# Kernel optimization log

Hardware: AMD Instinct MI355X
Metric: run time of the kernel (lower is better)

## Reference

```python
import jax, jax.numpy as jnp
import numpy as np


def setup_inputs() -> dict:
    key = jax.random.key(0)
    k1, k2, k3, k4 = jax.random.split(key, 4)
    B, T, N, C_IN, C_OUT, K = 32, 24, 1024, 64, 64, 3
    x = jax.random.normal(k1, (B, T, N, C_IN), dtype=jnp.float32)
    Tks = jax.random.normal(k2, (K, N, N), dtype=jnp.float32)
    # kaiming-uniform-ish init scale for Theta, small uniform bias
    bound_t = float(np.sqrt(6.0 / C_IN))
    Theta = jax.random.uniform(k3, (K, C_IN, C_OUT), dtype=jnp.float32,
                               minval=-bound_t, maxval=bound_t)
    bound_b = 1.0 / float(np.sqrt(C_IN))
    bias = jax.random.uniform(k4, (K, C_OUT), dtype=jnp.float32,
                              minval=-bound_b, maxval=bound_b)
    return {"x": x, "Tks": Tks, "Theta": Theta, "bias": bias}


def reference(x, Tks, Theta, bias):
    # torch.einsum('nn,btnc->btnc', T_k, x) extracts diag(T_k) and scales x per node.
    d = jnp.diagonal(Tks, axis1=1, axis2=2)  # [K, N]
    # sum_k diag(T_k) * x @ Theta_k  -> [B, T, N, C_OUT]
    out = jnp.einsum('kn,btnc,kco->btno', d, x, Theta)
    # each bias[k] is added once -> total additive term is sum over k
    out = out + jnp.sum(bias, axis=0)
    return out
```

## Files before the change

kernel.cpp:

```cpp
#include <hip/hip_runtime.h>


#define NNODES 1024
#define TILE_ROWS 64
#define NT 8
#define ROWS_PER_BLOCK (TILE_ROWS * NT)
#define NBLOCKS (786432 / ROWS_PER_BLOCK)

#define WS_W  0
#define WS_BS (24 * 1024)
#define WS_DV (24 * 1024 + 256)

typedef __attribute__((ext_vector_type(8))) short short8;
typedef __attribute__((ext_vector_type(4))) float f32x4;
typedef __attribute__((ext_vector_type(4))) int   i32x4;

__device__ __forceinline__ unsigned short f2bf(float f) {
    union { float f; unsigned u; } v; v.f = f;
    unsigned r = v.u + 0x7FFFu + ((v.u >> 16) & 1u);
    return (unsigned short)(r >> 16);
}

__device__ __forceinline__ int cvt_pk_bf16(float lo, float hi) {
    int r;
    asm("v_cvt_pk_bf16_f32 %0, %1, %2" : "=v"(r) : "v"(lo), "v"(hi));
    return r;
}

__device__ __forceinline__ void gload_lds16(const void* g, void* l) {
    __builtin_amdgcn_global_load_lds(
        (const __attribute__((address_space(1))) void*)g,
        (__attribute__((address_space(3))) void*)l,
        16, 0, 0);
}

__global__ void cheb_prep(const float* __restrict__ Tks,
                          const float* __restrict__ Theta,
                          const float* __restrict__ bias,
                          unsigned char* __restrict__ ws) {
    const int b = blockIdx.x;
    const int l = threadIdx.x;
    if (b < 24) {
        const int kc = b >> 3, h = (b >> 2) & 1, nb = b & 3;
        const int o  = nb * 16 + (l & 15);
        const int cb = h * 32 + (l >> 4) * 8;
        unsigned short* dst = (unsigned short*)(ws + WS_W) + ((size_t)b * 64 + l) * 8;
        #pragma unroll
        for (int j = 0; j < 8; ++j)
            dst[j] = f2bf(Theta[kc * 4096 + (cb + j) * 64 + o]);
    } else if (b < 40) {
        const int n = (b - 24) * 64 + l;
        const size_t dg = (size_t)n * (NNODES + 1);
        f32x4 v;
        v[0] = Tks[dg];
        v[1] = Tks[(size_t)NNODES * NNODES + dg];
        v[2] = Tks[(size_t)2 * NNODES * NNODES + dg];
        v[3] = 0.0f;
        *((f32x4*)(ws + WS_DV) + n) = v;
    } else {
        float* bs = (float*)(ws + WS_BS);
        bs[l] = bias[l] + bias[64 + l] + bias[128 + l];
    }
}

__global__ __launch_bounds__(256) void cheb_main(
    const float* __restrict__ x,
    const unsigned char* __restrict__ ws,
    float* __restrict__ out)
{
    __shared__ float xs[4][TILE_ROWS * 64];

    const int tid  = threadIdx.x;
    const int wave = tid >> 6;
    const int lane = tid & 63;
    const int lrow = lane & 15;
    const int lgrp = lane >> 4;
    const size_t rowbase = (size_t)blockIdx.x * ROWS_PER_BLOCK;

    const unsigned short* wimg = (const unsigned short*)(ws + WS_W);
    const float*          bsum = (const float*)(ws + WS_BS);
    const f32x4*          dvec = (const f32x4*)(ws + WS_DV);

    short8 wf[3][2][4];
    #pragma unroll
    for (int kc = 0; kc < 3; ++kc)
        #pragma unroll
        for (int h = 0; h < 2; ++h)
            #pragma unroll
            for (int nb = 0; nb < 4; ++nb)
                wf[kc][h][nb] = *(const short8*)(
                    wimg + ((size_t)(((kc * 2 + h) * 4 + nb) * 64 + lane)) * 8);

    f32x4 bs4[4];
    #pragma unroll
    for (int nb = 0; nb < 4; ++nb)
        bs4[nb] = *(const f32x4*)(bsum + nb * 16 + lgrp * 4);

    f32x4 dvr[NT];
    #pragma unroll
    for (int t = 0; t < NT; ++t)
        dvr[t] = dvec[(rowbase + t * TILE_ROWS + wave * 16 + lrow) & (NNODES - 1)];

#define STAGE(T) do { if ((T) < NT) {                                         \
        _Pragma("unroll")                                                     \
        for (int s = 0; s < 4; ++s) {                                         \
            const int u_ = wave * 4 + s;                                      \
            const int R_ = u_ * 4 + lgrp;                                     \
            const int c_ = (lrow * 16) ^ ((R_ & 7) << 4);                     \
            const char* g_ = (const char*)x +                                 \
                (((rowbase + (size_t)(T) * TILE_ROWS + R_) << 8) + c_);       \
            gload_lds16(g_, &xs[(T) & 3][u_ * 256]);                          \
        } } } while (0)

#define WAITV(N) do {                                                         \
        asm volatile("s_waitcnt vmcnt(" #N ")" ::: "memory");                 \
        __builtin_amdgcn_sched_barrier(0);                                    \
    } while (0)

#define BODY(T) do {                                                          \
        const int R = wave * 16 + lrow;                                       \
        const int m_ = (lrow & 7) << 4;                                       \
        const char* rowp = (const char*)&xs[(T) & 3][R * 64];                 \
        const int c00 = (lgrp * 32) ^ m_;                                     \
        const int c01 = (lgrp * 32 + 16) ^ m_;                                \
        const f32x4 x0 = *(const f32x4*)(rowp + c00);                         \
        const f32x4 x1 = *(const f32x4*)(rowp + c01);                         \
        const f32x4 x2 = *(const f32x4*)(rowp + 128 + c00);                   \
        const f32x4 x3 = *(const f32x4*)(rowp + 128 + c01);                   \
        const f32x4 dv = dvr[T];                                              \
        short8 xf[3][2];                                                      \
        _Pragma("unroll")                                                     \
        for (int kc = 0; kc < 3; ++kc) {                                      \
            const float dk = dv[kc];                                          \
            i32x4 r0, r1;                                                     \
            r0[0] = cvt_pk_bf16(dk * x0[0], dk * x0[1]);                      \
            r0[1] = cvt_pk_bf16(dk * x0[2], dk * x0[3]);                      \
            r0[2] = cvt_pk_bf16(dk * x1[0], dk * x1[1]);                      \
            r0[3] = cvt_pk_bf16(dk * x1[2], dk * x1[3]);                      \
            r1[0] = cvt_pk_bf16(dk * x2[0], dk * x2[1]);                      \
            r1[1] = cvt_pk_bf16(dk * x2[2], dk * x2[3]);                      \
            r1[2] = cvt_pk_bf16(dk * x3[0], dk * x3[1]);                      \
            r1[3] = cvt_pk_bf16(dk * x3[2], dk * x3[3]);                      \
            xf[kc][0] = __builtin_bit_cast(short8, r0);                       \
            xf[kc][1] = __builtin_bit_cast(short8, r1);                       \
        }                                                                     \
        f32x4 acc[4] = {f32x4{0,0,0,0}, f32x4{0,0,0,0},                       \
                        f32x4{0,0,0,0}, f32x4{0,0,0,0}};                      \
        _Pragma("unroll")                                                     \
        for (int kc = 0; kc < 3; ++kc)                                        \
            _Pragma("unroll")                                                 \
            for (int h = 0; h < 2; ++h)                                       \
                _Pragma("unroll")                                             \
                for (int nb = 0; nb < 4; ++nb)                                \
                    acc[nb] = __builtin_amdgcn_mfma_f32_16x16x32_bf16(        \
                        wf[kc][h][nb], xf[kc][h], acc[nb], 0, 0, 0);          \
        float* orow = out + (rowbase + (size_t)(T) * TILE_ROWS + R) * 64;     \
        _Pragma("unroll")                                                     \
        for (int nb = 0; nb < 4; ++nb) {                                      \
            f32x4 o4;                                                         \
            _Pragma("unroll")                                                 \
            for (int j = 0; j < 4; ++j) o4[j] = acc[nb][j] + bs4[nb][j];      \
            *(f32x4*)(orow + nb * 16 + lgrp * 4) = o4;                        \
        }                                                                     \
    } while (0)

    STAGE(0); STAGE(1); STAGE(2);
    STAGE(3);  WAITV(12); BODY(0);
    STAGE(4);  WAITV(16); BODY(1);
    STAGE(5);  WAITV(20); BODY(2);
    STAGE(6);  WAITV(24); BODY(3);
    STAGE(7);  WAITV(24); BODY(4);
    STAGE(8);  WAITV(20); BODY(5);
    STAGE(9);  WAITV(16); BODY(6);
    STAGE(10); WAITV(12); BODY(7);

#undef STAGE
#undef WAITV
#undef BODY
}

extern "C" void kernel_launch(void* const* d_in, const int* in_sizes, int n_in,
                              void* d_out, int out_size, void* d_ws, size_t ws_size,
                              hipStream_t stream) {
    const float* x     = (const float*)d_in[0];
    const float* Tks   = (const float*)d_in[1];
    const float* Theta = (const float*)d_in[2];
    const float* bias  = (const float*)d_in[3];
    float* out = (float*)d_out;
    unsigned char* ws = (unsigned char*)d_ws;

    hipLaunchKernelGGL(cheb_prep, dim3(41), dim3(64), 0, stream,
                       Tks, Theta, bias, ws);
    hipLaunchKernelGGL(cheb_main, dim3(NBLOCKS), dim3(256), 0, stream,
                       x, ws, out);
}
```

Baseline: 95.81 us.

## Split output columns across wave pairs with shared LDS tiles and barriers

The block grows from 256 to 512 threads. Each pair of waves now shares one 16-row x tile in LDS and splits the 64 output columns, so each wave holds half the Theta fragments and issues half the MFMAs. The LDS ring drops from four to three buffers, and the per-row diagonal scales are loaded asynchronously into LDS instead of per-thread registers. This lowers register pressure and raises occupancy for a bandwidth-bound kernel. In exchange it adds a workgroup barrier per tile, and both waves of a pair redo the same bf16 conversion.

```diff
diff --git a/kernel.cpp b/kernel.cpp
--- a/kernel.cpp
+++ b/kernel.cpp
@@ -63,71 +63,74 @@
     }
 }
 
-__global__ __launch_bounds__(256) void cheb_main(
+__global__ __launch_bounds__(512, 4) void cheb_main(
     const float* __restrict__ x,
     const unsigned char* __restrict__ ws,
     float* __restrict__ out)
 {
-    __shared__ float xs[4][TILE_ROWS * 64];
+    __shared__ float xs[3][TILE_ROWS * 64];
+    __shared__ __align__(16) float dvs[ROWS_PER_BLOCK][4];
 
     const int tid  = threadIdx.x;
     const int wave = tid >> 6;
     const int lane = tid & 63;
     const int lrow = lane & 15;
     const int lgrp = lane >> 4;
+    const int wr   = wave >> 1;
+    const int q    = wave & 1;
     const size_t rowbase = (size_t)blockIdx.x * ROWS_PER_BLOCK;
 
     const unsigned short* wimg = (const unsigned short*)(ws + WS_W);
     const float*          bsum = (const float*)(ws + WS_BS);
     const f32x4*          dvec = (const f32x4*)(ws + WS_DV);
 
-    short8 wf[3][2][4];
+    short8 wf[3][2][2];
     #pragma unroll
     for (int kc = 0; kc < 3; ++kc)
         #pragma unroll
         for (int h = 0; h < 2; ++h)
             #pragma unroll
-            for (int nb = 0; nb < 4; ++nb)
+            for (int nb = 0; nb < 2; ++nb)
                 wf[kc][h][nb] = *(const short8*)(
-                    wimg + ((size_t)(((kc * 2 + h) * 4 + nb) * 64 + lane)) * 8);
+                    wimg + ((size_t)(((kc * 2 + h) * 4 + q * 2 + nb) * 64 + lane)) * 8);
 
-    f32x4 bs4[4];
+    f32x4 bs4[2];
     #pragma unroll
-    for (int nb = 0; nb < 4; ++nb)
-        bs4[nb] = *(const f32x4*)(bsum + nb * 16 + lgrp * 4);
+    for (int nb = 0; nb < 2; ++nb)
+        bs4[nb] = *(const f32x4*)(bsum + q * 32 + nb * 16 + lgrp * 4);
 
-    f32x4 dvr[NT];
-    #pragma unroll
-    for (int t = 0; t < NT; ++t)
-        dvr[t] = dvec[(rowbase + t * TILE_ROWS + wave * 16 + lrow) & (NNODES - 1)];
+    gload_lds16((const char*)dvec + (((rowbase + wave * 64) & (NNODES - 1)) * 16 + lane * 16),
+                &dvs[wave * 64][0]);
 
 #define STAGE(T) do { if ((T) < NT) {                                         \
         _Pragma("unroll")                                                     \
-        for (int s = 0; s < 4; ++s) {                                         \
-            const int u_ = wave * 4 + s;                                      \
+        for (int s = 0; s < 2; ++s) {                                         \
+            const int u_ = wave * 2 + s;                                      \
             const int R_ = u_ * 4 + lgrp;                                     \
             const int c_ = (lrow * 16) ^ ((R_ & 7) << 4);                     \
             const char* g_ = (const char*)x +                                 \
                 (((rowbase + (size_t)(T) * TILE_ROWS + R_) << 8) + c_);       \
-            gload_lds16(g_, &xs[(T) & 3][u_ * 256]);                          \
+            gload_lds16(g_, (char*)&xs[(T) % 3][0] + u_ * 1024);              \
         } } } while (0)
 
 #define WAITV(N) do {                                                         \
         asm volatile("s_waitcnt vmcnt(" #N ")" ::: "memory");                 \
         __builtin_amdgcn_sched_barrier(0);                                    \
+        __builtin_amdgcn_s_barrier();                                         \
+        __builtin_amdgcn_sched_barrier(0);                                    \
     } while (0)
 
 #define BODY(T) do {                                                          \
-        const int R = wave * 16 + lrow;                                       \
+        const int R = wr * 16 + lrow;                                         \
         const int m_ = (lrow & 7) << 4;                                       \
-        const char* rowp = (const char*)&xs[(T) & 3][R * 64];                 \
+        const char* rowp = (const char*)&xs[(T) % 3][0] + R * 256;            \
         const int c00 = (lgrp * 32) ^ m_;                                     \
         const int c01 = (lgrp * 32 + 16) ^ m_;                                \
         const f32x4 x0 = *(const f32x4*)(rowp + c00);                         \
         const f32x4 x1 = *(const f32x4*)(rowp + c01);                         \
         const f32x4 x2 = *(const f32x4*)(rowp + 128 + c00);                   \
         const f32x4 x3 = *(const f32x4*)(rowp + 128 + c01);                   \
-        const f32x4 dv = dvr[T];                                              \
+        const f32x4 dv = *(const f32x4*)(&dvs[(T) * TILE_ROWS + R][0]);       \
         short8 xf[3][2];                                                      \
         _Pragma("unroll")                                                     \
         for (int kc = 0; kc < 3; ++kc) {                                      \
@@ -144,19 +147,19 @@
             xf[kc][0] = __builtin_bit_cast(short8, r0);                       \
             xf[kc][1] = __builtin_bit_cast(short8, r1);                       \
         }                                                                     \
-        f32x4 acc[4] = {f32x4{0,0,0,0}, f32x4{0,0,0,0},                       \
-                        f32x4{0,0,0,0}, f32x4{0,0,0,0}};                      \
+        f32x4 acc[2] = {f32x4{0,0,0,0}, f32x4{0,0,0,0}};                      \
         _Pragma("unroll")                                                     \
         for (int kc = 0; kc < 3; ++kc)                                        \
             _Pragma("unroll")                                                 \
             for (int h = 0; h < 2; ++h)                                       \
                 _Pragma("unroll")                                             \
-                for (int nb = 0; nb < 4; ++nb)                                \
+                for (int nb = 0; nb < 2; ++nb)                                \
                     acc[nb] = __builtin_amdgcn_mfma_f32_16x16x32_bf16(        \
                         wf[kc][h][nb], xf[kc][h], acc[nb], 0, 0, 0);          \
-        float* orow = out + (rowbase + (size_t)(T) * TILE_ROWS + R) * 64;     \
+        float* orow = out + (rowbase + (size_t)(T) * TILE_ROWS + R) * 64      \
+                          + q * 32;                                           \
         _Pragma("unroll")                                                     \
-        for (int nb = 0; nb < 4; ++nb) {                                      \
+        for (int nb = 0; nb < 2; ++nb) {                                      \
             f32x4 o4;                                                         \
             _Pragma("unroll")                                                 \
             for (int j = 0; j < 4; ++j) o4[j] = acc[nb][j] + bs4[nb][j];      \
@@ -164,15 +167,15 @@
         }                                                                     \
     } while (0)
 
-    STAGE(0); STAGE(1); STAGE(2);
-    STAGE(3);  WAITV(12); BODY(0);
-    STAGE(4);  WAITV(16); BODY(1);
-    STAGE(5);  WAITV(20); BODY(2);
-    STAGE(6);  WAITV(24); BODY(3);
-    STAGE(7);  WAITV(24); BODY(4);
-    STAGE(8);  WAITV(20); BODY(5);
-    STAGE(9);  WAITV(16); BODY(6);
-    STAGE(10); WAITV(12); BODY(7);
+    STAGE(0); STAGE(1);
+    WAITV(2); STAGE(2);  BODY(0);
+    WAITV(4); STAGE(3);  BODY(1);
+    WAITV(6); STAGE(4);  BODY(2);
+    WAITV(6); STAGE(5);  BODY(3);
+    WAITV(6); STAGE(6);  BODY(4);
+    WAITV(6); STAGE(7);  BODY(5);
+    WAITV(6); STAGE(8);  BODY(6);
+    WAITV(4); STAGE(9);  BODY(7);
 
 #undef STAGE
 #undef WAITV
@@ -191,6 +194,6 @@
 
     hipLaunchKernelGGL(cheb_prep, dim3(41), dim3(64), 0, stream,
                        Tks, Theta, bias, ws);
-    hipLaunchKernelGGL(cheb_main, dim3(NBLOCKS), dim3(256), 0, stream,
+    hipLaunchKernelGGL(cheb_main, dim3(NBLOCKS), dim3(512), 0, stream,
                        x, ws, out);
 }
```

New measurement: 90.30 us. 1.06x faster.
